# Optimization experiments

Measured on AMD Instinct MI355X. Metric: run time of the kernel, lower is better.

Reference implementation:

```python
import jax, jax.numpy as jnp
import numpy as np

N = 10000
K = 16
MEAN_NODES = 625.0  # N / K


def setup_inputs() -> dict:
    key = jax.random.key(0)
    k1, k2, k3 = jax.random.split(key, 3)
    # Y: soft partition assignments [N, K]; keep strictly positive so gamma > 0
    Y = jax.random.uniform(k1, (N, K), dtype=jnp.float32, minval=0.01, maxval=1.0)
    # A: dense adjacency / edge-weight matrix [N, N]
    A = jax.random.uniform(k2, (N, N), dtype=jnp.float32)
    # degree: per-node degree column vector [N, 1]
    degree = jax.random.uniform(k3, (N, 1), dtype=jnp.float32, minval=0.5, maxval=2.0)
    return {"Y": Y, "A": A, "degree": degree}


def reference(Y, A, degree):
    # gamma_k = sum_i Y[i,k] * degree[i]  -> [K, 1]
    gamma = Y.T @ degree                      # [K, 1]
    Yn = Y / gamma.reshape(1, K)              # divide column k by gamma_k, [N, K]
    # error_cut = sum_ij A_ij * (Yn @ (1 - Y^T))_ij
    error_cut = ((Yn @ (1.0 - Y.T)) * A).sum()
    # error_partition = sum_k (sum_i Y[i,k] - mean_nodes)^2
    col_sums = Y.sum(axis=0)                  # [K]
    error_partition = jnp.square(col_sums - MEAN_NODES).sum()
    return error_cut + error_partition
```

## Files before the change

### kernel.cpp

```cpp
#include <hip/hip_runtime.h>

#define N_NODES 10000
#define K_COLS 16
#define MEAN_NODES 625.0f

#define WS_PART_OFF 64
#define PREP_BLOCKS 40

typedef float vf4 __attribute__((ext_vector_type(4)));

__global__ __launch_bounds__(256) void prep_partial(const float* __restrict__ Y,
                                                    const float* __restrict__ deg,
                                                    float* __restrict__ ws) {
    const int b = blockIdx.x;
    const int t = threadIdx.x;
    const int i = b * 250 + t;
    const bool valid = (t < 250);

    float y[K_COLS];
    float d = 0.f;
    if (valid) {
        d = deg[i];
        const float4* yp = (const float4*)(Y + (size_t)i * K_COLS);
        *(float4*)(y + 0)  = yp[0];
        *(float4*)(y + 4)  = yp[1];
        *(float4*)(y + 8)  = yp[2];
        *(float4*)(y + 12) = yp[3];
    } else {
#pragma unroll
        for (int k = 0; k < K_COLS; ++k) y[k] = 0.f;
    }

    float g[K_COLS], c[K_COLS];
#pragma unroll
    for (int k = 0; k < K_COLS; ++k) { g[k] = y[k] * d; c[k] = y[k]; }

#pragma unroll
    for (int k = 0; k < K_COLS; ++k) {
        for (int off = 32; off > 0; off >>= 1) {
            g[k] += __shfl_down(g[k], off);
            c[k] += __shfl_down(c[k], off);
        }
    }

    __shared__ float red[4][32];
    const int wave = t >> 6, lane = t & 63;
    if (lane == 0) {
#pragma unroll
        for (int k = 0; k < K_COLS; ++k) {
            red[wave][k] = g[k];
            red[wave][K_COLS + k] = c[k];
        }
    }
    __syncthreads();

    if (t < 32) {
        float v = red[0][t] + red[1][t] + red[2][t] + red[3][t];
        ws[WS_PART_OFF + b * 32 + t] = v;
    }
}

__global__ __launch_bounds__(64) void prep_final(float* __restrict__ ws,
                                                 float* __restrict__ out) {
    const int t = threadIdx.x;
    if (t < 32) {
        float v = 0.f;
#pragma unroll
        for (int b = 0; b < PREP_BLOCKS; ++b) v += ws[WS_PART_OFF + b * 32 + t];
        if (t < 16) {
            ws[t] = 1.0f / v;
        } else {
            float dlt = v - MEAN_NODES;
            float sq = dlt * dlt;
            for (int off = 8; off > 0; off >>= 1) sq += __shfl_down(sq, off, 16);
            if (t == 16) out[0] = sq;
        }
    }
}

#define ROWS_PER_SEG 100
#define JT_WIDTH 1024

__device__ __forceinline__ void accum_row(const vf4 a, const float* __restrict__ ynrow,
                                          const float si,
                                          float d[4][K_COLS], float r[4]) {
    const float av0 = a.x, av1 = a.y, av2 = a.z, av3 = a.w;
    r[0] += av0 * si; r[1] += av1 * si; r[2] += av2 * si; r[3] += av3 * si;
    float yn[K_COLS];
    *(float4*)(yn + 0)  = *(const float4*)(ynrow + 0);
    *(float4*)(yn + 4)  = *(const float4*)(ynrow + 4);
    *(float4*)(yn + 8)  = *(const float4*)(ynrow + 8);
    *(float4*)(yn + 12) = *(const float4*)(ynrow + 12);
#pragma unroll
    for (int k = 0; k < K_COLS; ++k) {
        d[0][k] += av0 * yn[k];
        d[1][k] += av1 * yn[k];
        d[2][k] += av2 * yn[k];
        d[3][k] += av3 * yn[k];
    }
}

__global__ __launch_bounds__(256, 4) void gap_main(const float* __restrict__ A,
                                                   const float* __restrict__ Y,
                                                   const float* __restrict__ ws,
                                                   float* __restrict__ out) {
    __shared__ float YnL[ROWS_PER_SEG][K_COLS];
    __shared__ float sL[ROWS_PER_SEG];

    const int t = threadIdx.x;
    const int i0 = blockIdx.y * ROWS_PER_SEG;
    const int j0 = blockIdx.x * JT_WIDTH + (t << 2);
    const bool jvalid = j0 < N_NODES;
    const int jc = jvalid ? j0 : (N_NODES - 4);

    if (t < ROWS_PER_SEG) {
        const float* yrow = Y + (size_t)(i0 + t) * K_COLS;
        float yn[K_COLS];
        float s = 0.f;
#pragma unroll
        for (int k = 0; k < K_COLS; ++k) {
            yn[k] = yrow[k] * ws[k];
            s += yn[k];
        }
#pragma unroll
        for (int k = 0; k < K_COLS; ++k) YnL[t][k] = yn[k];
        sL[t] = s;
    }
    __syncthreads();

    float d[4][K_COLS];
    float r[4] = {0.f, 0.f, 0.f, 0.f};
#pragma unroll
    for (int jj = 0; jj < 4; ++jj)
#pragma unroll
        for (int k = 0; k < K_COLS; ++k) d[jj][k] = 0.f;

    const float* __restrict__ Ab = A + (size_t)i0 * N_NODES + jc;

    vf4 a0 = __builtin_nontemporal_load((const vf4*)(Ab));
    vf4 a1 = __builtin_nontemporal_load((const vf4*)(Ab + N_NODES));

#pragma unroll 1
    for (int ii = 0; ii < ROWS_PER_SEG; ii += 2) {
        const int n2 = (ii + 2 < ROWS_PER_SEG) ? ii + 2 : ROWS_PER_SEG - 1;
        const int n3 = (ii + 3 < ROWS_PER_SEG) ? ii + 3 : ROWS_PER_SEG - 1;
        const vf4 p0 = __builtin_nontemporal_load((const vf4*)(Ab + (size_t)n2 * N_NODES));
        const vf4 p1 = __builtin_nontemporal_load((const vf4*)(Ab + (size_t)n3 * N_NODES));

        accum_row(a0, &YnL[ii][0],     sL[ii],     d, r);
        accum_row(a1, &YnL[ii + 1][0], sL[ii + 1], d, r);

        a0 = p0; a1 = p1;
    }

    float partial = 0.f;
    if (jvalid) {
#pragma unroll
        for (int jj = 0; jj < 4; ++jj) {
            const float* yj = Y + (size_t)(j0 + jj) * K_COLS;
            float yv[K_COLS];
            *(float4*)(yv + 0)  = *(const float4*)(yj + 0);
            *(float4*)(yv + 4)  = *(const float4*)(yj + 4);
            *(float4*)(yv + 8)  = *(const float4*)(yj + 8);
            *(float4*)(yv + 12) = *(const float4*)(yj + 12);
            float dot = 0.f;
#pragma unroll
            for (int k = 0; k < K_COLS; ++k) dot += d[jj][k] * yv[k];
            partial += r[jj] - dot;
        }
    }

    for (int off = 32; off > 0; off >>= 1) partial += __shfl_down(partial, off);
    __shared__ float wpart[4];
    const int wave = t >> 6, lane = t & 63;
    if (lane == 0) wpart[wave] = partial;
    __syncthreads();
    if (t == 0)
        atomicAdd(out, (wpart[0] + wpart[1]) + (wpart[2] + wpart[3]));
}

extern "C" void kernel_launch(void* const* d_in, const int* in_sizes, int n_in,
                              void* d_out, int out_size, void* d_ws, size_t ws_size,
                              hipStream_t stream) {
    const float* Y   = (const float*)d_in[0];
    const float* A   = (const float*)d_in[1];
    const float* deg = (const float*)d_in[2];
    float* out = (float*)d_out;
    float* ws  = (float*)d_ws;

    hipLaunchKernelGGL(prep_partial, dim3(PREP_BLOCKS), dim3(256), 0, stream, Y, deg, ws);
    hipLaunchKernelGGL(prep_final, dim3(1), dim3(64), 0, stream, ws, out);
    hipLaunchKernelGGL(gap_main, dim3(10, 100), dim3(256), 0, stream, A, Y, ws, out);
}
```

Baseline: 504.0 us.

## Precompute normalized Y table and read it via wave-uniform scalar loads

Adds a yn_build kernel that writes Y scaled by the gamma reciprocals, plus the per-row sums, into the workspace. The main kernel then reads these rows through wave-uniform (readfirstlane) addresses so the compiler can use scalar loads, instead of building the table in LDS behind a block barrier. The last prefetch iteration is peeled out to drop the clamped index arithmetic. This removes LDS reads and the __syncthreads from the hot loop, at the cost of an extra kernel launch and dependence on scalar-cache bandwidth.

```diff
diff --git a/kernel.cpp b/kernel.cpp
--- a/kernel.cpp
+++ b/kernel.cpp
@@ -6,8 +6,12 @@
 
 #define WS_PART_OFF 64
 #define PREP_BLOCKS 40
+#define WS_YN_OFF 2048
+#define WS_S_OFF (WS_YN_OFF + N_NODES * K_COLS)
 
 typedef float vf4 __attribute__((ext_vector_type(4)));
+
+#define UNI(x) __builtin_amdgcn_readfirstlane(x)
 
 __global__ __launch_bounds__(256) void prep_partial(const float* __restrict__ Y,
                                                     const float* __restrict__ deg,
@@ -78,25 +82,54 @@
     }
 }
 
+__global__ __launch_bounds__(256) void yn_build(const float* __restrict__ Y,
+                                                float* ws) {
+    const int i = blockIdx.x * 256 + threadIdx.x;
+    if (i >= N_NODES) return;
+
+    float rg[K_COLS];
+#pragma unroll
+    for (int k = 0; k < K_COLS; ++k) rg[k] = ws[k];
+
+    float y[K_COLS];
+    const float4* yp = (const float4*)(Y + (size_t)i * K_COLS);
+    *(float4*)(y + 0)  = yp[0];
+    *(float4*)(y + 4)  = yp[1];
+    *(float4*)(y + 8)  = yp[2];
+    *(float4*)(y + 12) = yp[3];
+
+    float yn[K_COLS];
+    float s = 0.f;
+#pragma unroll
+    for (int k = 0; k < K_COLS; ++k) { yn[k] = y[k] * rg[k]; s += yn[k]; }
+
+    float4* o = (float4*)(ws + WS_YN_OFF + (size_t)i * K_COLS);
+    o[0] = *(float4*)(yn + 0);
+    o[1] = *(float4*)(yn + 4);
+    o[2] = *(float4*)(yn + 8);
+    o[3] = *(float4*)(yn + 12);
+    ws[WS_S_OFF + i] = s;
+}
+
 #define ROWS_PER_SEG 100
 #define JT_WIDTH 1024
 
-__device__ __forceinline__ void accum_row(const vf4 a, const float* __restrict__ ynrow,
+__device__ __forceinline__ vf4 ldA(const float* __restrict__ p, int lo) {
+    return __builtin_nontemporal_load((const vf4*)(p + lo));
+}
+
+__device__ __forceinline__ void accum_row(const vf4 a, const float* __restrict__ ynp,
                                           const float si,
                                           float d[4][K_COLS], float r[4]) {
     const float av0 = a.x, av1 = a.y, av2 = a.z, av3 = a.w;
     r[0] += av0 * si; r[1] += av1 * si; r[2] += av2 * si; r[3] += av3 * si;
-    float yn[K_COLS];
-    *(float4*)(yn + 0)  = *(const float4*)(ynrow + 0);
-    *(float4*)(yn + 4)  = *(const float4*)(ynrow + 4);
-    *(float4*)(yn + 8)  = *(const float4*)(ynrow + 8);
-    *(float4*)(yn + 12) = *(const float4*)(ynrow + 12);
 #pragma unroll
     for (int k = 0; k < K_COLS; ++k) {
-        d[0][k] += av0 * yn[k];
-        d[1][k] += av1 * yn[k];
-        d[2][k] += av2 * yn[k];
-        d[3][k] += av3 * yn[k];
+        const float yk = ynp[k];
+        d[0][k] += av0 * yk;
+        d[1][k] += av1 * yk;
+        d[2][k] += av2 * yk;
+        d[3][k] += av3 * yk;
     }
 }
 
@@ -104,29 +137,15 @@
                                                    const float* __restrict__ Y,
                                                    const float* __restrict__ ws,
                                                    float* __restrict__ out) {
-    __shared__ float YnL[ROWS_PER_SEG][K_COLS];
-    __shared__ float sL[ROWS_PER_SEG];
-
     const int t = threadIdx.x;
     const int i0 = blockIdx.y * ROWS_PER_SEG;
-    const int j0 = blockIdx.x * JT_WIDTH + (t << 2);
-    const bool jvalid = j0 < N_NODES;
-    const int jc = jvalid ? j0 : (N_NODES - 4);
-
-    if (t < ROWS_PER_SEG) {
-        const float* yrow = Y + (size_t)(i0 + t) * K_COLS;
-        float yn[K_COLS];
-        float s = 0.f;
-#pragma unroll
-        for (int k = 0; k < K_COLS; ++k) {
-            yn[k] = yrow[k] * ws[k];
-            s += yn[k];
-        }
-#pragma unroll
-        for (int k = 0; k < K_COLS; ++k) YnL[t][k] = yn[k];
-        sL[t] = s;
-    }
-    __syncthreads();
+    const int jblk = blockIdx.x * JT_WIDTH;
+    const int lane_j = jblk + (t << 2);
+    const bool jvalid = lane_j < N_NODES;
+    const int lo = jvalid ? (t << 2) : (N_NODES - 4 - jblk);
+
+    const float* __restrict__ yn_tab = ws + WS_YN_OFF;
+    const float* __restrict__ s_tab  = ws + WS_S_OFF;
 
     float d[4][K_COLS];
     float r[4] = {0.f, 0.f, 0.f, 0.f};
@@ -135,29 +154,36 @@
 #pragma unroll
         for (int k = 0; k < K_COLS; ++k) d[jj][k] = 0.f;
 
-    const float* __restrict__ Ab = A + (size_t)i0 * N_NODES + jc;
-
-    vf4 a0 = __builtin_nontemporal_load((const vf4*)(Ab));
-    vf4 a1 = __builtin_nontemporal_load((const vf4*)(Ab + N_NODES));
+    const float* __restrict__ Arow = A + (size_t)i0 * N_NODES + jblk;
+
+    vf4 a0 = ldA(Arow, lo);
+    vf4 a1 = ldA(Arow + N_NODES, lo);
 
 #pragma unroll 1
-    for (int ii = 0; ii < ROWS_PER_SEG; ii += 2) {
-        const int n2 = (ii + 2 < ROWS_PER_SEG) ? ii + 2 : ROWS_PER_SEG - 1;
-        const int n3 = (ii + 3 < ROWS_PER_SEG) ? ii + 3 : ROWS_PER_SEG - 1;
-        const vf4 p0 = __builtin_nontemporal_load((const vf4*)(Ab + (size_t)n2 * N_NODES));
-        const vf4 p1 = __builtin_nontemporal_load((const vf4*)(Ab + (size_t)n3 * N_NODES));
-
-        accum_row(a0, &YnL[ii][0],     sL[ii],     d, r);
-        accum_row(a1, &YnL[ii + 1][0], sL[ii + 1], d, r);
+    for (int ii = 0; ii < ROWS_PER_SEG - 2; ii += 2) {
+        const float* pp = Arow + (size_t)(ii + 2) * N_NODES;
+        const vf4 p0 = ldA(pp, lo);
+        const vf4 p1 = ldA(pp + N_NODES, lo);
+
+        const int ro = UNI((i0 + ii) * K_COLS);
+        const int rs = UNI(i0 + ii);
+        accum_row(a0, yn_tab + ro,          s_tab[rs],     d, r);
+        accum_row(a1, yn_tab + ro + K_COLS, s_tab[rs + 1], d, r);
 
         a0 = p0; a1 = p1;
+    }
+    {
+        const int ro = UNI((i0 + ROWS_PER_SEG - 2) * K_COLS);
+        const int rs = UNI(i0 + ROWS_PER_SEG - 2);
+        accum_row(a0, yn_tab + ro,          s_tab[rs],     d, r);
+        accum_row(a1, yn_tab + ro + K_COLS, s_tab[rs + 1], d, r);
     }
 
     float partial = 0.f;
     if (jvalid) {
 #pragma unroll
         for (int jj = 0; jj < 4; ++jj) {
-            const float* yj = Y + (size_t)(j0 + jj) * K_COLS;
+            const float* yj = Y + (size_t)(lane_j + jj) * K_COLS;
             float yv[K_COLS];
             *(float4*)(yv + 0)  = *(const float4*)(yj + 0);
             *(float4*)(yv + 4)  = *(const float4*)(yj + 4);
@@ -190,5 +216,6 @@
 
     hipLaunchKernelGGL(prep_partial, dim3(PREP_BLOCKS), dim3(256), 0, stream, Y, deg, ws);
     hipLaunchKernelGGL(prep_final, dim3(1), dim3(64), 0, stream, ws, out);
+    hipLaunchKernelGGL(yn_build, dim3((N_NODES + 255) / 256), dim3(256), 0, stream, Y, ws);
     hipLaunchKernelGGL(gap_main, dim3(10, 100), dim3(256), 0, stream, A, Y, ws, out);
 }
```

After: 503.8 us. No clear change (-0.1%).
